# Optimization experiments

Hardware: AMD Instinct MI355X
Metric: run time of the kernel (lower is better)

The kernel has to match this reference:

```python
import jax, jax.numpy as jnp
import numpy as np


def setup_inputs() -> dict:
    key = jax.random.key(0)
    ks = jax.random.split(key, 8)
    B, S, T, H, A = 4, 1024, 256, 512, 256
    return {
        "encoder_outputs": jax.random.normal(ks[0], (B, S, H), dtype=jnp.float32),
        "decoder_hidden": jax.random.normal(ks[1], (B, T, H), dtype=jnp.float32),
        "Wh": jax.random.normal(ks[2], (H, A), dtype=jnp.float32) * (1.0 / np.sqrt(H)),
        "bh": jax.random.normal(ks[3], (A,), dtype=jnp.float32) * 0.01,
        "Ws": jax.random.normal(ks[4], (H, A), dtype=jnp.float32) * (1.0 / np.sqrt(H)),
        "bs": jax.random.normal(ks[5], (A,), dtype=jnp.float32) * 0.01,
        "Wv": jax.random.normal(ks[6], (A, 1), dtype=jnp.float32) * (1.0 / np.sqrt(A)),
        "bv": jax.random.normal(ks[7], (1,), dtype=jnp.float32) * 0.01,
    }


def reference(encoder_outputs, decoder_hidden, Wh, bh, Ws, bs, Wv, bv):
    # encoder_outputs: [B, S, H], decoder_hidden: [B, T, H]
    eh = encoder_outputs @ Wh + bh          # [B, S, A]
    dh = decoder_hidden @ Ws + bs           # [B, T, A]
    # broadcast-add (torch's unsqueeze+repeat is just a broadcast), tanh, then v-projection
    energy = jnp.tanh(eh[:, None, :, :] + dh[:, :, None, :])  # [B, T, S, A]
    scores = jnp.einsum("btsa,a->bts", energy, Wv[:, 0]) + bv[0]  # [B, T, S]
    return jax.nn.softmax(scores, axis=2)
```

## Files before the change

kernel.cpp:

```cpp
#include <hip/hip_runtime.h>

#define B_ 4
#define S_ 1024
#define T_ 256
#define H_ 512
#define A_ 256
#define TT 4

typedef __attribute__((ext_vector_type(8))) short short8;
typedef __attribute__((ext_vector_type(4))) float f32x4;

__device__ __forceinline__ float ex2(float x)   { return __builtin_amdgcn_exp2f(x); }
__device__ __forceinline__ float rcpf_(float x) { return __builtin_amdgcn_rcpf(x); }

#define K2F 2.8853900817779268f
#define LOG2EF 1.4426950408889634f

__device__ __forceinline__ void split_bf16(float x, unsigned short& h, unsigned short& l)
{
    unsigned u = __float_as_uint(x);
    unsigned r = (u + 0x7FFFu + ((u >> 16) & 1u)) >> 16;
    h = (unsigned short)r;
    float hf = __uint_as_float(r << 16);
    float lo = x - hf;
    unsigned u2 = __float_as_uint(lo);
    l = (unsigned short)((u2 + 0x7FFFu + ((u2 >> 16) & 1u)) >> 16);
}

__global__ __launch_bounds__(256)
void prep_w(const float* __restrict__ Wh, const float* __restrict__ Wsm,
            unsigned short* __restrict__ WhTh, unsigned short* __restrict__ WhTl,
            unsigned short* __restrict__ WsTh, unsigned short* __restrict__ WsTl)
{
    __shared__ float lds[32][36];
    const int tid = threadIdx.x, bid = blockIdx.x;
    const int mat = bid >> 7, rem = bid & 127;
    const int k0 = (rem & 15) * 32, a0 = (rem >> 4) * 32;
    const float* W = mat ? Wsm : Wh;
    unsigned short* Oh = mat ? WsTh : WhTh;
    unsigned short* Ol = mat ? WsTl : WhTl;

    {
        int kl = tid >> 3, a4 = (tid & 7) * 4;
        float4 v = *(const float4*)&W[(size_t)(k0 + kl) * A_ + a0 + a4];
        lds[kl][a4] = v.x; lds[kl][a4 + 1] = v.y; lds[kl][a4 + 2] = v.z; lds[kl][a4 + 3] = v.w;
    }
    __syncthreads();
    {
        int al = tid >> 3, k4 = (tid & 7) * 4;
        unsigned short h[4], l[4];
        #pragma unroll
        for (int i = 0; i < 4; ++i) split_bf16(lds[k4 + i][al], h[i], l[i]);
        size_t o = (size_t)(a0 + al) * H_ + k0 + k4;
        *(ushort4*)&Oh[o] = make_ushort4(h[0], h[1], h[2], h[3]);
        *(ushort4*)&Ol[o] = make_ushort4(l[0], l[1], l[2], l[3]);
    }
}

__global__ __launch_bounds__(256)
void gemm_mfma(const float* __restrict__ enc, const float* __restrict__ dec,
               const unsigned short* __restrict__ WhTh, const unsigned short* __restrict__ WhTl,
               const unsigned short* __restrict__ WsTh, const unsigned short* __restrict__ WsTl,
               const float* __restrict__ bh, const float* __restrict__ bs,
               float* __restrict__ Ebuf, float* __restrict__ Dbuf)
{
    __shared__ short smem[8192];
    short* Ah = smem;
    short* Al = smem + 2048;
    short* Bh = smem + 4096;
    short* Bl = smem + 6144;

    const int tid = threadIdx.x, bid = blockIdx.x;
    const bool isE = bid < 256;
    int mb, nb;
    const float* Ag; const unsigned short* WTh; const unsigned short* WTl; const float* bias;
    if (isE) { mb = (bid & 63) * 64; nb = (bid >> 6) * 64; Ag = enc; WTh = WhTh; WTl = WhTl; bias = bh; }
    else { int b2 = bid - 256; mb = (b2 & 15) * 64; nb = (b2 >> 4) * 64; Ag = dec; WTh = WsTh; WTl = WsTl; bias = bs; }

    const int m_l = tid >> 2, q = tid & 3;
    const size_t arow = (size_t)(mb + m_l) * H_ + 8 * q;
    const size_t brow = (size_t)(nb + m_l) * H_ + 8 * q;
    const int woff = ((m_l >> 4) * 64 + (m_l & 15) + 16 * q) * 8;

    const int wave = tid >> 6, lane = tid & 63;
    const int wm = wave >> 1, wn = wave & 1;
    const int roffA = (2 * wm) * 512 + lane * 8;
    const int roffB = (2 * wn) * 512 + lane * 8;

    const int cl = lane & 15, rg = lane >> 4;
    const float bias0 = bias[nb + wn * 32 + cl];
    const float bias1 = bias[nb + wn * 32 + 16 + cl];

    f32x4 acc[2][2] = {};

    float4 aA = *(const float4*)&Ag[arow];
    float4 aB = *(const float4*)&Ag[arow + 4];
    short8 bHv = *(const short8*)&WTh[brow];
    short8 bLv = *(const short8*)&WTl[brow];

    for (int it = 0; it < 16; ++it) {
        __syncthreads();
        {
            float xs[8] = {aA.x, aA.y, aA.z, aA.w, aB.x, aB.y, aB.z, aB.w};
            short8 hv, lv;
            #pragma unroll
            for (int j = 0; j < 8; ++j) {
                unsigned short h, l; split_bf16(xs[j], h, l);
                hv[j] = (short)h; lv[j] = (short)l;
            }
            *(short8*)&Ah[woff] = hv;
            *(short8*)&Al[woff] = lv;
            *(short8*)&Bh[woff] = bHv;
            *(short8*)&Bl[woff] = bLv;
        }
        if (it < 15) {
            int kn = (it + 1) * 32;
            aA  = *(const float4*)&Ag[arow + kn];
            aB  = *(const float4*)&Ag[arow + kn + 4];
            bHv = *(const short8*)&WTh[brow + kn];
            bLv = *(const short8*)&WTl[brow + kn];
        }
        __syncthreads();
        short8 fAh0 = *(short8*)&Ah[roffA], fAh1 = *(short8*)&Ah[roffA + 512];
        short8 fAl0 = *(short8*)&Al[roffA], fAl1 = *(short8*)&Al[roffA + 512];
        short8 fBh0 = *(short8*)&Bh[roffB], fBh1 = *(short8*)&Bh[roffB + 512];
        short8 fBl0 = *(short8*)&Bl[roffB], fBl1 = *(short8*)&Bl[roffB + 512];
        acc[0][0] = __builtin_amdgcn_mfma_f32_16x16x32_bf16(fAh0, fBh0, acc[0][0], 0, 0, 0);
        acc[0][0] = __builtin_amdgcn_mfma_f32_16x16x32_bf16(fAh0, fBl0, acc[0][0], 0, 0, 0);
        acc[0][0] = __builtin_amdgcn_mfma_f32_16x16x32_bf16(fAl0, fBh0, acc[0][0], 0, 0, 0);
        acc[0][1] = __builtin_amdgcn_mfma_f32_16x16x32_bf16(fAh0, fBh1, acc[0][1], 0, 0, 0);
        acc[0][1] = __builtin_amdgcn_mfma_f32_16x16x32_bf16(fAh0, fBl1, acc[0][1], 0, 0, 0);
        acc[0][1] = __builtin_amdgcn_mfma_f32_16x16x32_bf16(fAl0, fBh1, acc[0][1], 0, 0, 0);
        acc[1][0] = __builtin_amdgcn_mfma_f32_16x16x32_bf16(fAh1, fBh0, acc[1][0], 0, 0, 0);
        acc[1][0] = __builtin_amdgcn_mfma_f32_16x16x32_bf16(fAh1, fBl0, acc[1][0], 0, 0, 0);
        acc[1][0] = __builtin_amdgcn_mfma_f32_16x16x32_bf16(fAl1, fBh0, acc[1][0], 0, 0, 0);
        acc[1][1] = __builtin_amdgcn_mfma_f32_16x16x32_bf16(fAh1, fBh1, acc[1][1], 0, 0, 0);
        acc[1][1] = __builtin_amdgcn_mfma_f32_16x16x32_bf16(fAh1, fBl1, acc[1][1], 0, 0, 0);
        acc[1][1] = __builtin_amdgcn_mfma_f32_16x16x32_bf16(fAl1, fBh1, acc[1][1], 0, 0, 0);
    }

    #pragma unroll
    for (int mf = 0; mf < 2; ++mf) {
        const int mg = mb + wm * 32 + mf * 16 + rg * 4;
        #pragma unroll
        for (int nf = 0; nf < 2; ++nf) {
            const int a = nb + wn * 32 + nf * 16 + cl;
            const float bb = nf ? bias1 : bias0;
            f32x4 ac = acc[mf][nf];
            float4 st;
            st.x = ex2((ac[0] + bb) * K2F);
            st.y = ex2((ac[1] + bb) * K2F);
            st.z = ex2((ac[2] + bb) * K2F);
            st.w = ex2((ac[3] + bb) * K2F);
            if (isE) {
                const int b = mg >> 10, s = mg & 1023;
                *(float4*)&Ebuf[(((size_t)b * A_ + a) << 10) + s] = st;
            } else {
                Dbuf[(size_t)(mg + 0) * A_ + a] = st.x;
                Dbuf[(size_t)(mg + 1) * A_ + a] = st.y;
                Dbuf[(size_t)(mg + 2) * A_ + a] = st.z;
                Dbuf[(size_t)(mg + 3) * A_ + a] = st.w;
            }
        }
    }
}

__device__ __forceinline__ void pair_acc(float e1, float e2, float d1, float d2,
                                         float w1, float w2, float& acc)
{
    float q1  = fmaf(e1, d1, 1.0f);
    float q2  = fmaf(e2, d2, 1.0f);
    float num = fmaf(w1, q2, w2 * q1);
    acc = fmaf(num, rcpf_(q1 * q2), acc);
}

__global__ __launch_bounds__(1024)
void score_softmax(const float* __restrict__ E, const float* __restrict__ D,
                   const float* __restrict__ Wv, float* __restrict__ out)
{
    const int tid = threadIdx.x;
    const int b  = blockIdx.x >> 6;
    const int t0 = (blockIdx.x & 63) * TT;

    __shared__ float redm[TT][16];
    __shared__ float reds[TT][16];

    const float* Eb = E + (size_t)b * A_ * S_ + tid;
    const float* Dg = D + ((size_t)b * T_ + t0) * A_;

    float acc[TT] = {};
    float evA[8], evB[8];
    #pragma unroll
    for (int u = 0; u < 8; ++u) evA[u] = Eb[(size_t)u * S_];

#define CHUNK8(EV, A0)                                                        \
    {                                                                         \
        float4 w0 = *(const float4*)&Wv[(A0)];                                \
        float4 w1 = *(const float4*)&Wv[(A0) + 4];                            \
        _Pragma("unroll")                                                     \
        for (int t = 0; t < TT; ++t) {                                        \
            float4 d0 = *(const float4*)&Dg[t * A_ + (A0)];                   \
            float4 d1 = *(const float4*)&Dg[t * A_ + (A0) + 4];               \
            pair_acc(EV[0], EV[1], d0.x, d0.y, w0.x, w0.y, acc[t]);           \
            pair_acc(EV[2], EV[3], d0.z, d0.w, w0.z, w0.w, acc[t]);           \
            pair_acc(EV[4], EV[5], d1.x, d1.y, w1.x, w1.y, acc[t]);           \
            pair_acc(EV[6], EV[7], d1.z, d1.w, w1.z, w1.w, acc[t]);           \
        }                                                                     \
    }

    for (int a0 = 0; a0 < A_; a0 += 16) {
        #pragma unroll
        for (int u = 0; u < 8; ++u) evB[u] = Eb[(size_t)(a0 + 8 + u) * S_];
        CHUNK8(evA, a0);
        if (a0 + 16 < A_) {
            #pragma unroll
            for (int u = 0; u < 8; ++u) evA[u] = Eb[(size_t)(a0 + 16 + u) * S_];
        }
        CHUNK8(evB, a0 + 8);
    }
#undef CHUNK8

    const int lane = tid & 63, wid = tid >> 6;
    float sc[TT];
    #pragma unroll
    for (int t = 0; t < TT; ++t) sc[t] = -2.0f * acc[t];

    #pragma unroll
    for (int t = 0; t < TT; ++t) {
        float mx = sc[t];
        #pragma unroll
        for (int off = 32; off > 0; off >>= 1) mx = fmaxf(mx, __shfl_xor(mx, off, 64));
        if (lane == 0) redm[t][wid] = mx;
    }
    __syncthreads();

    float mrow[TT];
    #pragma unroll
    for (int t = 0; t < TT; ++t) {
        float m = redm[t][0];
        #pragma unroll
        for (int i = 1; i < 16; ++i) m = fmaxf(m, redm[t][i]);
        mrow[t] = m;
    }

    #pragma unroll
    for (int t = 0; t < TT; ++t) {
        sc[t] = ex2((sc[t] - mrow[t]) * LOG2EF);
        float s = sc[t];
        #pragma unroll
        for (int off = 32; off > 0; off >>= 1) s += __shfl_xor(s, off, 64);
        if (lane == 0) reds[t][wid] = s;
    }
    __syncthreads();

    #pragma unroll
    for (int t = 0; t < TT; ++t) {
        float ssum = reds[t][0];
        #pragma unroll
        for (int i = 1; i < 16; ++i) ssum += reds[t][i];
        float inv = 1.0f / ssum;
        out[((size_t)b * T_ + (t0 + t)) * S_ + tid] = sc[t] * inv;
    }
}

extern "C" void kernel_launch(void* const* d_in, const int* in_sizes, int n_in,
                              void* d_out, int out_size, void* d_ws, size_t ws_size,
                              hipStream_t stream)
{
    const float* enc = (const float*)d_in[0];
    const float* dec = (const float*)d_in[1];
    const float* Wh  = (const float*)d_in[2];
    const float* bh  = (const float*)d_in[3];
    const float* Wsm = (const float*)d_in[4];
    const float* bs  = (const float*)d_in[5];
    const float* Wv  = (const float*)d_in[6];

    float* Ebuf = (float*)d_ws;
    float* Dbuf = Ebuf + (size_t)B_ * A_ * S_;
    unsigned short* wt = (unsigned short*)(Dbuf + (size_t)B_ * T_ * A_);
    unsigned short* WhTh = wt;
    unsigned short* WhTl = wt + 131072;
    unsigned short* WsTh = wt + 262144;
    unsigned short* WsTl = wt + 393216;

    prep_w<<<256, 256, 0, stream>>>(Wh, Wsm, WhTh, WhTl, WsTh, WsTl);
    gemm_mfma<<<320, 256, 0, stream>>>(enc, dec, WhTh, WhTl, WsTh, WsTl,
                                       bh, bs, Ebuf, Dbuf);
    score_softmax<<<B_ * (T_ / TT), 1024, 0, stream>>>(Ebuf, Dbuf, Wv, (float*)d_out);
}
```

Before: 58.37 us.

## Retile score kernel to 2 rows x 2 columns per thread with LDS-staged D and Wv

The score/softmax kernel now uses 512-thread blocks that each handle 2 decoder rows, and every thread computes 2 adjacent source positions using float2 loads of E and float2 stores. D rows and Wv are staged once into shared memory and read as vectors from LDS, replacing the per-thread global loads. The grid doubles to 512 blocks for better CU coverage. The cost is more E re-reads across blocks (2 rows per block instead of 4) and extra LDS traffic.

```diff
diff --git a/kernel.cpp b/kernel.cpp
--- a/kernel.cpp
+++ b/kernel.cpp
@@ -5,7 +5,6 @@
 #define T_ 256
 #define H_ 512
 #define A_ 256
-#define TT 4
 
 typedef __attribute__((ext_vector_type(8))) short short8;
 typedef __attribute__((ext_vector_type(4))) float f32x4;
@@ -174,79 +173,107 @@
     acc = fmaf(num, rcpf_(q1 * q2), acc);
 }
 
-__global__ __launch_bounds__(1024)
+#define LD8(dst, srcp)                                                     \
+    { float4 x_ = *(const float4*)(srcp); float4 y_ = *(const float4*)((srcp) + 4); \
+      dst[0] = x_.x; dst[1] = x_.y; dst[2] = x_.z; dst[3] = x_.w;          \
+      dst[4] = y_.x; dst[5] = y_.y; dst[6] = y_.z; dst[7] = y_.w; }
+
+__global__ __launch_bounds__(512)
 void score_softmax(const float* __restrict__ E, const float* __restrict__ D,
                    const float* __restrict__ Wv, float* __restrict__ out)
 {
     const int tid = threadIdx.x;
-    const int b  = blockIdx.x >> 6;
-    const int t0 = (blockIdx.x & 63) * TT;
-
-    __shared__ float redm[TT][16];
-    __shared__ float reds[TT][16];
-
-    const float* Eb = E + (size_t)b * A_ * S_ + tid;
-    const float* Dg = D + ((size_t)b * T_ + t0) * A_;
-
-    float acc[TT] = {};
-    float evA[8], evB[8];
-    #pragma unroll
-    for (int u = 0; u < 8; ++u) evA[u] = Eb[(size_t)u * S_];
-
-#define CHUNK8(EV, A0)                                                        \
-    {                                                                         \
-        float4 w0 = *(const float4*)&Wv[(A0)];                                \
-        float4 w1 = *(const float4*)&Wv[(A0) + 4];                            \
-        _Pragma("unroll")                                                     \
-        for (int t = 0; t < TT; ++t) {                                        \
-            float4 d0 = *(const float4*)&Dg[t * A_ + (A0)];                   \
-            float4 d1 = *(const float4*)&Dg[t * A_ + (A0) + 4];               \
-            pair_acc(EV[0], EV[1], d0.x, d0.y, w0.x, w0.y, acc[t]);           \
-            pair_acc(EV[2], EV[3], d0.z, d0.w, w0.z, w0.w, acc[t]);           \
-            pair_acc(EV[4], EV[5], d1.x, d1.y, w1.x, w1.y, acc[t]);           \
-            pair_acc(EV[6], EV[7], d1.z, d1.w, w1.z, w1.w, acc[t]);           \
-        }                                                                     \
+    const int b  = blockIdx.x >> 7;
+    const int t0 = (blockIdx.x & 127) * 2;
+
+    __shared__ float Dsh[2][A_];
+    __shared__ float Wsh[A_];
+    __shared__ float redm[2][8];
+    __shared__ float reds[2][8];
+
+    if (tid < 128) {
+        int r = tid >> 6, c4 = (tid & 63) << 2;
+        *(float4*)&Dsh[r][c4] = *(const float4*)&D[((size_t)b * T_ + t0 + r) * A_ + c4];
+    } else if (tid < 192) {
+        int c4 = (tid - 128) << 2;
+        *(float4*)&Wsh[c4] = *(const float4*)&Wv[c4];
+    }
+    __syncthreads();
+
+    const int s0 = tid << 1;
+    const float* Eb = E + (size_t)b * A_ * S_ + s0;
+
+    float acc[2][2] = {};
+    float2 evA[8], evB[8];
+    float dA[2][8], dB[2][8], wA[8], wB[8];
+
+    #pragma unroll
+    for (int u = 0; u < 8; ++u) evA[u] = *(const float2*)&Eb[(size_t)u * S_];
+    #pragma unroll
+    for (int t = 0; t < 2; ++t) LD8(dA[t], &Dsh[t][0]);
+    LD8(wA, &Wsh[0]);
+
+#define HALF(EV, DD, WW)                                                        \
+    _Pragma("unroll")                                                           \
+    for (int t = 0; t < 2; ++t) {                                               \
+        _Pragma("unroll")                                                       \
+        for (int p = 0; p < 4; ++p) {                                           \
+            float d1 = DD[t][2 * p], d2 = DD[t][2 * p + 1];                     \
+            float w1 = WW[2 * p],    w2 = WW[2 * p + 1];                        \
+            pair_acc(EV[2 * p].x, EV[2 * p + 1].x, d1, d2, w1, w2, acc[t][0]);  \
+            pair_acc(EV[2 * p].y, EV[2 * p + 1].y, d1, d2, w1, w2, acc[t][1]);  \
+        }                                                                       \
     }
 
     for (int a0 = 0; a0 < A_; a0 += 16) {
         #pragma unroll
-        for (int u = 0; u < 8; ++u) evB[u] = Eb[(size_t)(a0 + 8 + u) * S_];
-        CHUNK8(evA, a0);
+        for (int u = 0; u < 8; ++u) evB[u] = *(const float2*)&Eb[(size_t)(a0 + 8 + u) * S_];
+        #pragma unroll
+        for (int t = 0; t < 2; ++t) LD8(dB[t], &Dsh[t][a0 + 8]);
+        LD8(wB, &Wsh[a0 + 8]);
+        HALF(evA, dA, wA);
         if (a0 + 16 < A_) {
             #pragma unroll
-            for (int u = 0; u < 8; ++u) evA[u] = Eb[(size_t)(a0 + 16 + u) * S_];
+            for (int u = 0; u < 8; ++u) evA[u] = *(const float2*)&Eb[(size_t)(a0 + 16 + u) * S_];
+            #pragma unroll
+            for (int t = 0; t < 2; ++t) LD8(dA[t], &Dsh[t][a0 + 16]);
+            LD8(wA, &Wsh[a0 + 16]);
         }
-        CHUNK8(evB, a0 + 8);
-    }
-#undef CHUNK8
+        HALF(evB, dB, wB);
+    }
+#undef HALF
 
     const int lane = tid & 63, wid = tid >> 6;
-    float sc[TT];
-    #pragma unroll
-    for (int t = 0; t < TT; ++t) sc[t] = -2.0f * acc[t];
-
-    #pragma unroll
-    for (int t = 0; t < TT; ++t) {
-        float mx = sc[t];
+    float sc[2][2];
+    #pragma unroll
+    for (int t = 0; t < 2; ++t) {
+        sc[t][0] = -2.0f * acc[t][0];
+        sc[t][1] = -2.0f * acc[t][1];
+    }
+
+    #pragma unroll
+    for (int t = 0; t < 2; ++t) {
+        float mx = fmaxf(sc[t][0], sc[t][1]);
         #pragma unroll
         for (int off = 32; off > 0; off >>= 1) mx = fmaxf(mx, __shfl_xor(mx, off, 64));
         if (lane == 0) redm[t][wid] = mx;
     }
     __syncthreads();
 
-    float mrow[TT];
-    #pragma unroll
-    for (int t = 0; t < TT; ++t) {
+    float mrow[2];
+    #pragma unroll
+    for (int t = 0; t < 2; ++t) {
         float m = redm[t][0];
         #pragma unroll
-        for (int i = 1; i < 16; ++i) m = fmaxf(m, redm[t][i]);
+        for (int i = 1; i < 8; ++i) m = fmaxf(m, redm[t][i]);
         mrow[t] = m;
     }
 
     #pragma unroll
-    for (int t = 0; t < TT; ++t) {
-        sc[t] = ex2((sc[t] - mrow[t]) * LOG2EF);
-        float s = sc[t];
+    for (int t = 0; t < 2; ++t) {
+        sc[t][0] = ex2((sc[t][0] - mrow[t]) * LOG2EF);
+        sc[t][1] = ex2((sc[t][1] - mrow[t]) * LOG2EF);
+        float s = sc[t][0] + sc[t][1];
         #pragma unroll
         for (int off = 32; off > 0; off >>= 1) s += __shfl_xor(s, off, 64);
         if (lane == 0) reds[t][wid] = s;
@@ -254,12 +281,13 @@
     __syncthreads();
 
     #pragma unroll
-    for (int t = 0; t < TT; ++t) {
+    for (int t = 0; t < 2; ++t) {
         float ssum = reds[t][0];
         #pragma unroll
-        for (int i = 1; i < 16; ++i) ssum += reds[t][i];
+        for (int i = 1; i < 8; ++i) ssum += reds[t][i];
         float inv = 1.0f / ssum;
-        out[((size_t)b * T_ + (t0 + t)) * S_ + tid] = sc[t] * inv;
+        float2 o = make_float2(sc[t][0] * inv, sc[t][1] * inv);
+        *(float2*)&out[((size_t)b * T_ + (t0 + t)) * S_ + s0] = o;
     }
 }
 
@@ -286,5 +314,5 @@
     prep_w<<<256, 256, 0, stream>>>(Wh, Wsm, WhTh, WhTl, WsTh, WsTl);
     gemm_mfma<<<320, 256, 0, stream>>>(enc, dec, WhTh, WhTl, WsTh, WsTl,
                                        bh, bs, Ebuf, Dbuf);
-    score_softmax<<<B_ * (T_ / TT), 1024, 0, stream>>>(Ebuf, Dbuf, Wv, (float*)d_out);
-}
+    score_softmax<<<B_ * (T_ / 2), 512, 0, stream>>>(Ebuf, Dbuf, Wv, (float*)d_out);
+}
```

After: 66.77 us. +14.4%, slower.

## Split score over A halves with packed math, merge partials in separate softmax kernel

Applied to the files above, without the earlier changes.

The fused score+softmax kernel is replaced by two kernels. The first splits the A reduction into two halves across blocks, processes 2 t-rows × 2 s-values per thread using packed f32x2 FMAs, and combines four terms per reciprocal instead of two. It also stages D and Wv in LDS. Partial sums go to the output buffer and a workspace buffer, then a second kernel adds them and runs the softmax without max subtraction, relying on bounded scores. This adds parallelism and cuts rcp count, at the cost of an extra launch and extra global traffic for the partials.

```diff
diff --git a/kernel.cpp b/kernel.cpp
--- a/kernel.cpp
+++ b/kernel.cpp
@@ -5,16 +5,16 @@
 #define T_ 256
 #define H_ 512
 #define A_ 256
-#define TT 4
 
 typedef __attribute__((ext_vector_type(8))) short short8;
 typedef __attribute__((ext_vector_type(4))) float f32x4;
+typedef __attribute__((ext_vector_type(2))) float f32x2;
 
 __device__ __forceinline__ float ex2(float x)   { return __builtin_amdgcn_exp2f(x); }
 __device__ __forceinline__ float rcpf_(float x) { return __builtin_amdgcn_rcpf(x); }
+__device__ __forceinline__ f32x2 splat2(float v) { f32x2 r; r.x = v; r.y = v; return r; }
 
 #define K2F 2.8853900817779268f
-#define LOG2EF 1.4426950408889634f
 
 __device__ __forceinline__ void split_bf16(float x, unsigned short& h, unsigned short& l)
 {
@@ -165,102 +165,111 @@
     }
 }
 
-__device__ __forceinline__ void pair_acc(float e1, float e2, float d1, float d2,
-                                         float w1, float w2, float& acc)
-{
-    float q1  = fmaf(e1, d1, 1.0f);
-    float q2  = fmaf(e2, d2, 1.0f);
-    float num = fmaf(w1, q2, w2 * q1);
-    acc = fmaf(num, rcpf_(q1 * q2), acc);
-}
-
-__global__ __launch_bounds__(1024)
-void score_softmax(const float* __restrict__ E, const float* __restrict__ D,
-                   const float* __restrict__ Wv, float* __restrict__ out)
+__device__ __forceinline__ void four_acc(const f32x2* ev, f32x2 d01, f32x2 d23,
+                                         f32x2 w01, f32x2 w23, f32x2& acc)
+{
+    const f32x2 one = {1.0f, 1.0f};
+    f32x2 q0 = __builtin_elementwise_fma(ev[0], splat2(d01.x), one);
+    f32x2 q1 = __builtin_elementwise_fma(ev[1], splat2(d01.y), one);
+    f32x2 q2 = __builtin_elementwise_fma(ev[2], splat2(d23.x), one);
+    f32x2 q3 = __builtin_elementwise_fma(ev[3], splat2(d23.y), one);
+    f32x2 q01 = q0 * q1, q23 = q2 * q3;
+    f32x2 t01 = __builtin_elementwise_fma(splat2(w01.x), q1, splat2(w01.y) * q0);
+    f32x2 t23 = __builtin_elementwise_fma(splat2(w23.x), q3, splat2(w23.y) * q2);
+    f32x2 num = __builtin_elementwise_fma(t01, q23, t23 * q01);
+    f32x2 den = q01 * q23;
+    f32x2 r; r.x = rcpf_(den.x); r.y = rcpf_(den.y);
+    acc = __builtin_elementwise_fma(num, r, acc);
+}
+
+#define LOADG(EV, DT, WW, G)                                            \
+    { int ab_ = 4 * (G);                                                \
+      EV[0] = *(const f32x2*)&Eb[(size_t)(ab_ + 0) << 10];              \
+      EV[1] = *(const f32x2*)&Eb[(size_t)(ab_ + 1) << 10];              \
+      EV[2] = *(const f32x2*)&Eb[(size_t)(ab_ + 2) << 10];              \
+      EV[3] = *(const f32x2*)&Eb[(size_t)(ab_ + 3) << 10];              \
+      DT[0] = *(const f32x2*)&Dsh[0][ab_];                              \
+      DT[1] = *(const f32x2*)&Dsh[0][ab_ + 2];                          \
+      DT[2] = *(const f32x2*)&Dsh[1][ab_];                              \
+      DT[3] = *(const f32x2*)&Dsh[1][ab_ + 2];                          \
+      WW[0] = *(const f32x2*)&Wsh[ab_];                                 \
+      WW[1] = *(const f32x2*)&Wsh[ab_ + 2]; }
+
+__global__ __launch_bounds__(512, 6)
+void score_partial(const float* __restrict__ E, const float* __restrict__ D,
+                   const float* __restrict__ Wv,
+                   float* __restrict__ P0, float* __restrict__ P1)
 {
     const int tid = threadIdx.x;
-    const int b  = blockIdx.x >> 6;
-    const int t0 = (blockIdx.x & 63) * TT;
-
-    __shared__ float redm[TT][16];
-    __shared__ float reds[TT][16];
-
-    const float* Eb = E + (size_t)b * A_ * S_ + tid;
-    const float* Dg = D + ((size_t)b * T_ + t0) * A_;
-
-    float acc[TT] = {};
-    float evA[8], evB[8];
+    const int bid = blockIdx.x;
+    const int b   = bid >> 8;
+    const int rem = bid & 255;
+    const int h   = rem & 1;
+    const int t0  = (rem >> 1) * 2;
+    const int abase = h * 128;
+
+    __shared__ float Dsh[2][128];
+    __shared__ float Wsh[128];
+
+    if (tid < 64) {
+        int r = tid >> 5, c4 = (tid & 31) << 2;
+        *(float4*)&Dsh[r][c4] = *(const float4*)&D[((size_t)b * T_ + t0 + r) * A_ + abase + c4];
+    } else if (tid < 96) {
+        int c4 = (tid - 64) << 2;
+        *(float4*)&Wsh[c4] = *(const float4*)&Wv[abase + c4];
+    }
+    __syncthreads();
+
+    const int s0 = tid << 1;
+    const float* Eb = E + ((size_t)b * A_ + abase) * S_ + s0;
+
+    f32x2 acc0 = {0.0f, 0.0f}, acc1 = {0.0f, 0.0f};
+    f32x2 evA[4], evB[4], dA[4], dB[4], wA[2], wB[2];
+
+    LOADG(evA, dA, wA, 0);
+    for (int g = 0; g < 32; g += 2) {
+        LOADG(evB, dB, wB, g + 1);
+        four_acc(evA, dA[0], dA[1], wA[0], wA[1], acc0);
+        four_acc(evA, dA[2], dA[3], wA[0], wA[1], acc1);
+        if (g + 2 < 32) LOADG(evA, dA, wA, g + 2);
+        four_acc(evB, dB[0], dB[1], wB[0], wB[1], acc0);
+        four_acc(evB, dB[2], dB[3], wB[0], wB[1], acc1);
+    }
+
+    float* Pd = h ? P1 : P0;
+    *(f32x2*)&Pd[((size_t)b * T_ + t0)     * S_ + s0] = acc0;
+    *(f32x2*)&Pd[((size_t)b * T_ + t0 + 1) * S_ + s0] = acc1;
+}
+#undef LOADG
+
+__global__ __launch_bounds__(256)
+void merge_softmax(const float* __restrict__ P1, float* __restrict__ outp)
+{
+    const int row = blockIdx.x;
+    const int tid = threadIdx.x;
+    const int lane = tid & 63, wid = tid >> 6;
+    __shared__ float red[4];
+
+    float* o = outp + (size_t)row * S_;
+    const float* p1 = P1 + (size_t)row * S_;
+    const int s4 = tid << 2;
+
+    float4 a = *(const float4*)&o[s4];
+    float4 c = *(const float4*)&p1[s4];
+    float e0 = ex2((a.x + c.x) * -K2F);
+    float e1 = ex2((a.y + c.y) * -K2F);
+    float e2 = ex2((a.z + c.z) * -K2F);
+    float e3 = ex2((a.w + c.w) * -K2F);
+
+    float ssum = (e0 + e1) + (e2 + e3);
     #pragma unroll
-    for (int u = 0; u < 8; ++u) evA[u] = Eb[(size_t)u * S_];
-
-#define CHUNK8(EV, A0)                                                        \
-    {                                                                         \
-        float4 w0 = *(const float4*)&Wv[(A0)];                                \
-        float4 w1 = *(const float4*)&Wv[(A0) + 4];                            \
-        _Pragma("unroll")                                                     \
-        for (int t = 0; t < TT; ++t) {                                        \
-            float4 d0 = *(const float4*)&Dg[t * A_ + (A0)];                   \
-            float4 d1 = *(const float4*)&Dg[t * A_ + (A0) + 4];               \
-            pair_acc(EV[0], EV[1], d0.x, d0.y, w0.x, w0.y, acc[t]);           \
-            pair_acc(EV[2], EV[3], d0.z, d0.w, w0.z, w0.w, acc[t]);           \
-            pair_acc(EV[4], EV[5], d1.x, d1.y, w1.x, w1.y, acc[t]);           \
-            pair_acc(EV[6], EV[7], d1.z, d1.w, w1.z, w1.w, acc[t]);           \
-        }                                                                     \
-    }
-
-    for (int a0 = 0; a0 < A_; a0 += 16) {
-        #pragma unroll
-        for (int u = 0; u < 8; ++u) evB[u] = Eb[(size_t)(a0 + 8 + u) * S_];
-        CHUNK8(evA, a0);
-        if (a0 + 16 < A_) {
-            #pragma unroll
-            for (int u = 0; u < 8; ++u) evA[u] = Eb[(size_t)(a0 + 16 + u) * S_];
-        }
-        CHUNK8(evB, a0 + 8);
-    }
-#undef CHUNK8
-
-    const int lane = tid & 63, wid = tid >> 6;
-    float sc[TT];
-    #pragma unroll
-    for (int t = 0; t < TT; ++t) sc[t] = -2.0f * acc[t];
-
-    #pragma unroll
-    for (int t = 0; t < TT; ++t) {
-        float mx = sc[t];
-        #pragma unroll
-        for (int off = 32; off > 0; off >>= 1) mx = fmaxf(mx, __shfl_xor(mx, off, 64));
-        if (lane == 0) redm[t][wid] = mx;
-    }
+    for (int off = 32; off > 0; off >>= 1) ssum += __shfl_xor(ssum, off, 64);
+    if (lane == 0) red[wid] = ssum;
     __syncthreads();
-
-    float mrow[TT];
-    #pragma unroll
-    for (int t = 0; t < TT; ++t) {
-        float m = redm[t][0];
-        #pragma unroll
-        for (int i = 1; i < 16; ++i) m = fmaxf(m, redm[t][i]);
-        mrow[t] = m;
-    }
-
-    #pragma unroll
-    for (int t = 0; t < TT; ++t) {
-        sc[t] = ex2((sc[t] - mrow[t]) * LOG2EF);
-        float s = sc[t];
-        #pragma unroll
-        for (int off = 32; off > 0; off >>= 1) s += __shfl_xor(s, off, 64);
-        if (lane == 0) reds[t][wid] = s;
-    }
-    __syncthreads();
-
-    #pragma unroll
-    for (int t = 0; t < TT; ++t) {
-        float ssum = reds[t][0];
-        #pragma unroll
-        for (int i = 1; i < 16; ++i) ssum += reds[t][i];
-        float inv = 1.0f / ssum;
-        out[((size_t)b * T_ + (t0 + t)) * S_ + tid] = sc[t] * inv;
-    }
+    float tot = (red[0] + red[1]) + (red[2] + red[3]);
+    float inv = 1.0f / tot;
+
+    *(float4*)&o[s4] = make_float4(e0 * inv, e1 * inv, e2 * inv, e3 * inv);
 }
 
 extern "C" void kernel_launch(void* const* d_in, const int* in_sizes, int n_in,
@@ -282,9 +291,12 @@
     unsigned short* WhTl = wt + 131072;
     unsigned short* WsTh = wt + 262144;
     unsigned short* WsTl = wt + 393216;
+    float* P1 = (float*)(wt + 524288);
+    float* P0 = (float*)d_out;
 
     prep_w<<<256, 256, 0, stream>>>(Wh, Wsm, WhTh, WhTl, WsTh, WsTl);
     gemm_mfma<<<320, 256, 0, stream>>>(enc, dec, WhTh, WhTl, WsTh, WsTl,
                                        bh, bs, Ebuf, Dbuf);
-    score_softmax<<<B_ * (T_ / TT), 1024, 0, stream>>>(Ebuf, Dbuf, Wv, (float*)d_out);
-}
+    score_partial<<<B_ * 256, 512, 0, stream>>>(Ebuf, Dbuf, Wv, P0, P1);
+    merge_softmax<<<B_ * T_, 256, 0, stream>>>(P1, (float*)d_out);
+}
```

Measured after the change: 65.57 us. +12.3%, slower.

## Split score kernel across A per wave and reduce partial scores through LDS

Applied to the files above, without the earlier changes.

The score kernel is reorganised so that each wave owns a 16-wide slice of the attention dimension and each lane handles 16 sequence positions, with the D and Wv slices held in registers. Per-wave partial scores are then summed into a padded LDS buffer in a 16-step serialized loop. The softmax also drops the max-subtraction pass, relying on scores being bounded. The aim is to cut repeated D/Wv loads and strided per-element E loads, at the cost of heavy register pressure (about 144 live floats under a 1024-thread launch bound, so spills are possible) and a barrier-heavy LDS reduction.

```diff
diff --git a/kernel.cpp b/kernel.cpp
--- a/kernel.cpp
+++ b/kernel.cpp
@@ -5,7 +5,6 @@
 #define T_ 256
 #define H_ 512
 #define A_ 256
-#define TT 4
 
 typedef __attribute__((ext_vector_type(8))) short short8;
 typedef __attribute__((ext_vector_type(4))) float f32x4;
@@ -14,7 +13,6 @@
 __device__ __forceinline__ float rcpf_(float x) { return __builtin_amdgcn_rcpf(x); }
 
 #define K2F 2.8853900817779268f
-#define LOG2EF 1.4426950408889634f
 
 __device__ __forceinline__ void split_bf16(float x, unsigned short& h, unsigned short& l)
 {
@@ -165,102 +163,98 @@
     }
 }
 
-__device__ __forceinline__ void pair_acc(float e1, float e2, float d1, float d2,
-                                         float w1, float w2, float& acc)
-{
-    float q1  = fmaf(e1, d1, 1.0f);
-    float q2  = fmaf(e2, d2, 1.0f);
-    float num = fmaf(w1, q2, w2 * q1);
-    acc = fmaf(num, rcpf_(q1 * q2), acc);
-}
-
 __global__ __launch_bounds__(1024)
-void score_softmax(const float* __restrict__ E, const float* __restrict__ D,
-                   const float* __restrict__ Wv, float* __restrict__ out)
-{
-    const int tid = threadIdx.x;
-    const int b  = blockIdx.x >> 6;
-    const int t0 = (blockIdx.x & 63) * TT;
-
-    __shared__ float redm[TT][16];
-    __shared__ float reds[TT][16];
-
-    const float* Eb = E + (size_t)b * A_ * S_ + tid;
-    const float* Dg = D + ((size_t)b * T_ + t0) * A_;
-
-    float acc[TT] = {};
-    float evA[8], evB[8];
-    #pragma unroll
-    for (int u = 0; u < 8; ++u) evA[u] = Eb[(size_t)u * S_];
-
-#define CHUNK8(EV, A0)                                                        \
-    {                                                                         \
-        float4 w0 = *(const float4*)&Wv[(A0)];                                \
-        float4 w1 = *(const float4*)&Wv[(A0) + 4];                            \
-        _Pragma("unroll")                                                     \
-        for (int t = 0; t < TT; ++t) {                                        \
-            float4 d0 = *(const float4*)&Dg[t * A_ + (A0)];                   \
-            float4 d1 = *(const float4*)&Dg[t * A_ + (A0) + 4];               \
-            pair_acc(EV[0], EV[1], d0.x, d0.y, w0.x, w0.y, acc[t]);           \
-            pair_acc(EV[2], EV[3], d0.z, d0.w, w0.z, w0.w, acc[t]);           \
-            pair_acc(EV[4], EV[5], d1.x, d1.y, w1.x, w1.y, acc[t]);           \
-            pair_acc(EV[6], EV[7], d1.z, d1.w, w1.z, w1.w, acc[t]);           \
-        }                                                                     \
-    }
-
-    for (int a0 = 0; a0 < A_; a0 += 16) {
-        #pragma unroll
-        for (int u = 0; u < 8; ++u) evB[u] = Eb[(size_t)(a0 + 8 + u) * S_];
-        CHUNK8(evA, a0);
-        if (a0 + 16 < A_) {
+void score_fused(const float* __restrict__ E, const float* __restrict__ D,
+                 const float* __restrict__ Wv, float* __restrict__ outp)
+{
+    const int tid  = threadIdx.x;
+    const int b    = blockIdx.x >> 6;
+    const int t0   = (blockIdx.x & 63) << 2;
+    const int wv   = __builtin_amdgcn_readfirstlane(tid >> 6);
+    const int lane = tid & 63;
+    const int abase = wv << 4;
+
+    __shared__ float sc[4 * 1152];
+    __shared__ float red[4][4];
+
+    for (int i = tid; i < 4 * 1152; i += 1024) sc[i] = 0.0f;
+
+    float sd[4][16], sw[16];
+    #pragma unroll
+    for (int t = 0; t < 4; ++t)
+        #pragma unroll
+        for (int i = 0; i < 16; ++i)
+            sd[t][i] = D[((size_t)b * T_ + t0 + t) * A_ + abase + i];
+    #pragma unroll
+    for (int i = 0; i < 16; ++i) sw[i] = Wv[abase + i];
+
+    const float* Eb = E + (((size_t)b * A_ + abase) << 10) + (lane << 2);
+    float acc[4][16] = {};
+
+    #pragma unroll
+    for (int p = 0; p < 8; ++p) {
+        const float* r0 = Eb + (size_t)(2 * p) * S_;
+        const float* r1 = r0 + S_;
+        #pragma unroll
+        for (int j = 0; j < 4; ++j) {
+            float4 e0 = *(const float4*)&r0[j * 256];
+            float4 e1 = *(const float4*)&r1[j * 256];
+            const float* e0f = (const float*)&e0;
+            const float* e1f = (const float*)&e1;
             #pragma unroll
-            for (int u = 0; u < 8; ++u) evA[u] = Eb[(size_t)(a0 + 16 + u) * S_];
-        }
-        CHUNK8(evB, a0 + 8);
-    }
-#undef CHUNK8
-
-    const int lane = tid & 63, wid = tid >> 6;
-    float sc[TT];
-    #pragma unroll
-    for (int t = 0; t < TT; ++t) sc[t] = -2.0f * acc[t];
-
-    #pragma unroll
-    for (int t = 0; t < TT; ++t) {
-        float mx = sc[t];
-        #pragma unroll
-        for (int off = 32; off > 0; off >>= 1) mx = fmaxf(mx, __shfl_xor(mx, off, 64));
-        if (lane == 0) redm[t][wid] = mx;
-    }
+            for (int t = 0; t < 4; ++t) {
+                const float d0 = sd[t][2 * p], d1 = sd[t][2 * p + 1];
+                #pragma unroll
+                for (int k = 0; k < 4; ++k) {
+                    float q0 = fmaf(e0f[k], d0, 1.0f);
+                    float q1 = fmaf(e1f[k], d1, 1.0f);
+                    float num = fmaf(sw[2 * p], q1, sw[2 * p + 1] * q0);
+                    acc[t][j * 4 + k] = fmaf(num, rcpf_(q0 * q1), acc[t][j * 4 + k]);
+                }
+            }
+        }
+    }
+
     __syncthreads();
-
-    float mrow[TT];
-    #pragma unroll
-    for (int t = 0; t < TT; ++t) {
-        float m = redm[t][0];
-        #pragma unroll
-        for (int i = 1; i < 16; ++i) m = fmaxf(m, redm[t][i]);
-        mrow[t] = m;
-    }
-
-    #pragma unroll
-    for (int t = 0; t < TT; ++t) {
-        sc[t] = ex2((sc[t] - mrow[t]) * LOG2EF);
-        float s = sc[t];
-        #pragma unroll
-        for (int off = 32; off > 0; off >>= 1) s += __shfl_xor(s, off, 64);
-        if (lane == 0) reds[t][wid] = s;
-    }
+    for (int w = 0; w < 16; ++w) {
+        if (wv == w) {
+            #pragma unroll
+            for (int t = 0; t < 4; ++t)
+                #pragma unroll
+                for (int j = 0; j < 4; ++j) {
+                    int s  = (j << 8) + (lane << 2);
+                    int ps = s + (s >> 3);
+                    float4 cur = *(float4*)&sc[t * 1152 + ps];
+                    cur.x += acc[t][j * 4 + 0];
+                    cur.y += acc[t][j * 4 + 1];
+                    cur.z += acc[t][j * 4 + 2];
+                    cur.w += acc[t][j * 4 + 3];
+                    *(float4*)&sc[t * 1152 + ps] = cur;
+                }
+        }
+        __syncthreads();
+    }
+
+    const int t  = tid >> 8;
+    const int ii = tid & 255;
+    const int s4 = ii << 2;
+    const int ps = s4 + (s4 >> 3);
+    float4 v = *(float4*)&sc[t * 1152 + ps];
+    float e0 = ex2(v.x * -K2F);
+    float e1 = ex2(v.y * -K2F);
+    float e2 = ex2(v.z * -K2F);
+    float e3 = ex2(v.w * -K2F);
+
+    float ssum = (e0 + e1) + (e2 + e3);
+    #pragma unroll
+    for (int off = 32; off > 0; off >>= 1) ssum += __shfl_xor(ssum, off, 64);
+    if (lane == 0) red[t][(tid >> 6) & 3] = ssum;
     __syncthreads();
-
-    #pragma unroll
-    for (int t = 0; t < TT; ++t) {
-        float ssum = reds[t][0];
-        #pragma unroll
-        for (int i = 1; i < 16; ++i) ssum += reds[t][i];
-        float inv = 1.0f / ssum;
-        out[((size_t)b * T_ + (t0 + t)) * S_ + tid] = sc[t] * inv;
-    }
+    float tot = (red[t][0] + red[t][1]) + (red[t][2] + red[t][3]);
+    float inv = 1.0f / tot;
+
+    *(float4*)&outp[(((size_t)b * T_ + t0 + t) << 10) + s4] =
+        make_float4(e0 * inv, e1 * inv, e2 * inv, e3 * inv);
 }
 
 extern "C" void kernel_launch(void* const* d_in, const int* in_sizes, int n_in,
@@ -275,9 +269,10 @@
     const float* bs  = (const float*)d_in[5];
     const float* Wv  = (const float*)d_in[6];
 
-    float* Ebuf = (float*)d_ws;
-    float* Dbuf = Ebuf + (size_t)B_ * A_ * S_;
-    unsigned short* wt = (unsigned short*)(Dbuf + (size_t)B_ * T_ * A_);
+    char* ws = (char*)d_ws;
+    float* Ebuf = (float*)ws;
+    float* Dbuf = (float*)(ws + (4 << 20));
+    unsigned short* wt = (unsigned short*)(ws + (5 << 20));
     unsigned short* WhTh = wt;
     unsigned short* WhTl = wt + 131072;
     unsigned short* WsTh = wt + 262144;
@@ -286,5 +281,5 @@
     prep_w<<<256, 256, 0, stream>>>(Wh, Wsm, WhTh, WhTl, WsTh, WsTl);
     gemm_mfma<<<320, 256, 0, stream>>>(enc, dec, WhTh, WhTl, WsTh, WsTl,
                                        bh, bs, Ebuf, Dbuf);
-    score_softmax<<<B_ * (T_ / TT), 1024, 0, stream>>>(Ebuf, Dbuf, Wv, (float*)d_out);
-}
+    score_fused<<<B_ * (T_ / 4), 1024, 0, stream>>>(Ebuf, Dbuf, Wv, (float*)d_out);
+}
```

Result: slower. 110.9 us (+90.0%).
